# Kernel optimization log

Measured on AMD Instinct MI355X. Metric: run time of the kernel, lower is better.

Reference implementation:

```python
import jax, jax.numpy as jnp
import numpy as np

M = 8192  # output rows (size[0])


def setup_inputs() -> dict:
    key = jax.random.key(0)
    k1, k2, k3 = jax.random.split(key, 3)
    nnz = 2097152
    ids = jax.random.randint(k1, (2, nnz), 0, 8192, dtype=jnp.int64)  # [2, nnz] COO (row, col)
    vals = jax.random.normal(k2, (nnz,), dtype=jnp.float32) * 0.02
    x = jax.random.normal(k3, (8192, 128), dtype=jnp.float32)  # [N, B]
    return {"ids": ids, "vals": vals, "x": x}


def reference(ids, vals, x):
    # torch.sparse.mm(W, x) with W = coo(ids, vals, (M, N)).coalesce():
    # coalescing sums duplicate (row, col) entries, which segment_sum also does,
    # so the math is identical without explicitly deduplicating.
    rows = ids[0]  # [nnz]
    cols = ids[1]  # [nnz]
    contrib = vals[:, None] * x[cols]               # [nnz, B] gather + scale
    out = jax.ops.segment_sum(contrib, rows, num_segments=M)  # [M, B] scatter-add
    return out
```

## Files before the change

kernel.cpp:

```cpp
#include <hip/hip_runtime.h>
#include <hip/hip_bf16.h>


#define M_ROWS 8192
#define B_COLS 128
#define NG   256
#define CHK  8192
#define NBK  512
#define CAP  5120

__device__ inline unsigned int f2bf(float f) {
    unsigned int u = __float_as_uint(f);
    return (u + 0x7fffu + ((u >> 16) & 1u)) >> 16;
}
__global__ void __launch_bounds__(256) convx_kernel(const float* __restrict__ x,
                                                    uint4* __restrict__ xb) {
    int i = blockIdx.x * 256 + threadIdx.x;
    const float4* p = (const float4*)x + (size_t)i * 2;
    float4 a = p[0], b = p[1];
    uint4 o;
    o.x = f2bf(a.x) | (f2bf(a.y) << 16);
    o.y = f2bf(a.z) | (f2bf(a.w) << 16);
    o.z = f2bf(b.x) | (f2bf(b.y) << 16);
    o.w = f2bf(b.z) | (f2bf(b.w) << 16);
    xb[i] = o;
}

__global__ void __launch_bounds__(256) histT_kernel(const int* __restrict__ rows, int nnz,
                                                    int* __restrict__ perHistT) {
    __shared__ int h[NBK];
    int t = threadIdx.x, g = blockIdx.x;
    for (int i = t; i < NBK; i += 256) h[i] = 0;
    __syncthreads();
    int s = g * CHK, e = min(s + CHK, nnz);
    for (int i = s + t; i < e; i += 256) atomicAdd(&h[rows[i] >> 4], 1);
    __syncthreads();
    for (int b = t; b < NBK; b += 256) perHistT[(size_t)b * NG + g] = h[b];
}

__global__ void __launch_bounds__(512) chunkscan_kernel(int* __restrict__ perHistT,
                                                        int* __restrict__ totals) {
    int wave = threadIdx.x >> 6, lane = threadIdx.x & 63;
    int b = blockIdx.x * 8 + wave;
    int4* p = (int4*)(perHistT + (size_t)b * NG) + lane;
    int4 c = *p;
    int s = c.x + c.y + c.z + c.w;
    int incl = s;
#pragma unroll
    for (int d = 1; d < 64; d <<= 1) {
        int up = __shfl_up(incl, d, 64);
        if (lane >= d) incl += up;
    }
    int base = incl - s;
    int4 o;
    o.x = base;
    o.y = base + c.x;
    o.z = o.y + c.y;
    o.w = o.z + c.z;
    *p = o;
    if (lane == 63) totals[b] = incl;
}

__global__ void __launch_bounds__(512) scanbk_kernel(const int* __restrict__ totals, int nnz,
                                                     int* __restrict__ bucketStart) {
    __shared__ int tsh[NBK];
    __shared__ int gbase[64];
    int b = threadIdx.x;
    tsh[b] = totals[b];
    __syncthreads();
    if (b < 64) {
        int gs = 0;
#pragma unroll
        for (int k = 0; k < 8; ++k) gs += tsh[b * 8 + k];
        gbase[b] = gs;
    }
    __syncthreads();
    if (b == 0) {
        int acc = 0;
        for (int i = 0; i < 64; ++i) { int c = gbase[i]; gbase[i] = acc; acc += c; }
    }
    __syncthreads();
    int off = gbase[b >> 3];
    for (int k = (b & ~7); k < b; ++k) off += tsh[k];
    bucketStart[b] = off;
    if (b == 0) bucketStart[NBK] = nnz;
}

__global__ void __launch_bounds__(1024) scatter_kernel(const int* __restrict__ rows,
                                                       const int* __restrict__ cols,
                                                       const float* __restrict__ vals,
                                                       int nnz,
                                                       const int* __restrict__ perHistT,
                                                       const int* __restrict__ bucketStart,
                                                       int2* __restrict__ pairs) {
    __shared__ int2 stage[CHK];
    __shared__ int hist[NBK];
    __shared__ int binStart[NBK];
    __shared__ int destB[NBK];
    __shared__ int gbase[64];
    int t = threadIdx.x, g = blockIdx.x;
    int s = g * CHK, e = min(s + CHK, nnz);
    int cnt = e - s;

    int   rr[CHK / 1024];
    int   cc[CHK / 1024];
    float vv[CHK / 1024];
    for (int i = t; i < NBK; i += 1024) hist[i] = 0;
    __syncthreads();
#pragma unroll
    for (int k = 0; k < CHK / 1024; ++k) {
        int i = s + t + k * 1024;
        if (i < e) {
            rr[k] = rows[i];
            cc[k] = cols[i];
            vv[k] = vals[i];
            atomicAdd(&hist[rr[k] >> 4], 1);
        } else rr[k] = -1;
    }
    __syncthreads();
    if (t < 64) {
        int gs = 0;
#pragma unroll
        for (int k = 0; k < 8; ++k) gs += hist[t * 8 + k];
        gbase[t] = gs;
    }
    __syncthreads();
    if (t == 0) {
        int acc = 0;
        for (int i = 0; i < 64; ++i) { int c = gbase[i]; gbase[i] = acc; acc += c; }
    }
    __syncthreads();
    if (t < NBK) {
        int off = gbase[t >> 3];
        for (int k = (t & ~7); k < t; ++k) off += hist[k];
        binStart[t] = off;
        destB[t] = bucketStart[t] + perHistT[(size_t)t * NG + g] - off;
    }
    __syncthreads();
    if (t < NBK) hist[t] = binStart[t];
    __syncthreads();
#pragma unroll
    for (int k = 0; k < CHK / 1024; ++k) {
        if (rr[k] >= 0) {
            int pos = atomicAdd(&hist[rr[k] >> 4], 1);
            stage[pos] = make_int2((rr[k] << 13) | cc[k], __float_as_int(vv[k]));
        }
    }
    __syncthreads();
#pragma unroll
    for (int k = 0; k < CHK / 1024; ++k) {
        int i = t + k * 1024;
        if (i < cnt) {
            int2 en = stage[i];
            int b = en.x >> 17;
            pairs[destB[b] + i] = make_int2(en.x & 0x1FFFF, en.y);
        }
    }
}

__global__ void __launch_bounds__(1024) sortspmm_kernel(const int2* __restrict__ pairs,
                                                        const int* __restrict__ bucketStart,
                                                        const unsigned short* __restrict__ xb,
                                                        float* __restrict__ out) {
    __shared__ int2 sorted[CAP];
    __shared__ int h16w[16 * 16];
    __shared__ int h16tot[16];
    __shared__ int rs[17];
    int t = threadIdx.x;
    int bkt = blockIdx.x;
    int segS = bucketStart[bkt];
    int n = bucketStart[bkt + 1] - segS;
    int nc = min(n, CAP);
    int wave = t >> 6, lane = t & 63;
    if (t < 256) h16w[t] = 0;
    __syncthreads();

    int2 buf[5];
#pragma unroll
    for (int k = 0; k < 5; ++k) {
        int i = t + 1024 * k;
        if (i < nc) {
            long long m = __builtin_nontemporal_load((const long long*)pairs + (segS + i));
            int2 en;
            en.x = (int)m;
            en.y = (int)(m >> 32);
            buf[k] = en;
            atomicAdd(&h16w[wave * 16 + ((en.x >> 13) & 15)], 1);
        }
    }
    __syncthreads();
    if (t < 16) {
        int acc = 0;
#pragma unroll
        for (int w = 0; w < 16; ++w) {
            int c = h16w[w * 16 + t];
            h16w[w * 16 + t] = acc;
            acc += c;
        }
        h16tot[t] = acc;
    }
    __syncthreads();
    if (t == 0) {
        int acc = 0;
#pragma unroll
        for (int j = 0; j < 16; ++j) { rs[j] = acc; acc += h16tot[j]; }
        rs[16] = acc;
    }
    __syncthreads();
    if (t < 256) {
        int w = t >> 4, b = t & 15;
        h16w[t] = rs[b] + h16w[w * 16 + b];
    }
    __syncthreads();
#pragma unroll
    for (int k = 0; k < 5; ++k) {
        int i = t + 1024 * k;
        if (i < nc) {
            int2 en = buf[k];
            int pos = atomicAdd(&h16w[wave * 16 + ((en.x >> 13) & 15)], 1);
            sorted[pos] = make_int2(en.x & 8191, en.y);
        }
    }
    __syncthreads();

    int g = lane >> 4, l16 = lane & 15;
    const unsigned short* xbl = xb + l16 * 8;
    int b0 = rs[wave], e0 = rs[wave + 1];
    float acc[8];
#pragma unroll
    for (int k = 0; k < 8; ++k) acc[k] = 0.f;

    for (int i = b0; i < e0; i += 16) {
        int i0 = i + g, i1 = i0 + 4, i2 = i0 + 8, i3 = i0 + 12;
        int2 ea = (i0 < e0) ? sorted[i0] : make_int2(0, 0);
        int2 eb = (i1 < e0) ? sorted[i1] : make_int2(0, 0);
        int2 ec = (i2 < e0) ? sorted[i2] : make_int2(0, 0);
        int2 ed = (i3 < e0) ? sorted[i3] : make_int2(0, 0);
        float va = (i0 < e0) ? __int_as_float(ea.y) : 0.f;
        float vb = (i1 < e0) ? __int_as_float(eb.y) : 0.f;
        float vc = (i2 < e0) ? __int_as_float(ec.y) : 0.f;
        float vd = (i3 < e0) ? __int_as_float(ed.y) : 0.f;
        const uint4 qa = *(const uint4*)(xbl + (size_t)ea.x * B_COLS);
        const uint4 qb = *(const uint4*)(xbl + (size_t)eb.x * B_COLS);
        const uint4 qc = *(const uint4*)(xbl + (size_t)ec.x * B_COLS);
        const uint4 qd = *(const uint4*)(xbl + (size_t)ed.x * B_COLS);
#pragma unroll
        for (int k = 0; k < 4; ++k) {
            unsigned int w = (&qa.x)[k];
            acc[2 * k]     = fmaf(va, __uint_as_float(w << 16), acc[2 * k]);
            acc[2 * k + 1] = fmaf(va, __uint_as_float(w & 0xffff0000u), acc[2 * k + 1]);
        }
#pragma unroll
        for (int k = 0; k < 4; ++k) {
            unsigned int w = (&qb.x)[k];
            acc[2 * k]     = fmaf(vb, __uint_as_float(w << 16), acc[2 * k]);
            acc[2 * k + 1] = fmaf(vb, __uint_as_float(w & 0xffff0000u), acc[2 * k + 1]);
        }
#pragma unroll
        for (int k = 0; k < 4; ++k) {
            unsigned int w = (&qc.x)[k];
            acc[2 * k]     = fmaf(vc, __uint_as_float(w << 16), acc[2 * k]);
            acc[2 * k + 1] = fmaf(vc, __uint_as_float(w & 0xffff0000u), acc[2 * k + 1]);
        }
#pragma unroll
        for (int k = 0; k < 4; ++k) {
            unsigned int w = (&qd.x)[k];
            acc[2 * k]     = fmaf(vd, __uint_as_float(w << 16), acc[2 * k]);
            acc[2 * k + 1] = fmaf(vd, __uint_as_float(w & 0xffff0000u), acc[2 * k + 1]);
        }
    }
    for (int i = CAP; i < n; ++i) {
        int2 en = pairs[segS + i];
        if (((en.x >> 13) & 15) == wave) {
            float v = (g == 0) ? __int_as_float(en.y) : 0.f;
            const uint4 q = *(const uint4*)(xbl + (size_t)(en.x & 8191) * B_COLS);
#pragma unroll
            for (int k = 0; k < 4; ++k) {
                unsigned int w = (&q.x)[k];
                acc[2 * k]     = fmaf(v, __uint_as_float(w << 16), acc[2 * k]);
                acc[2 * k + 1] = fmaf(v, __uint_as_float(w & 0xffff0000u), acc[2 * k + 1]);
            }
        }
    }
#pragma unroll
    for (int k = 0; k < 8; ++k) {
        acc[k] += __shfl_xor(acc[k], 16, 64);
        acc[k] += __shfl_xor(acc[k], 32, 64);
    }
    if (lane < 16) {
        float* op = out + ((size_t)(bkt * 16 + wave)) * B_COLS + l16 * 8;
        *(float4*)op       = make_float4(acc[0], acc[1], acc[2], acc[3]);
        *((float4*)op + 1) = make_float4(acc[4], acc[5], acc[6], acc[7]);
    }
}

__global__ void atomic_spmm_kernel(const int* __restrict__ rows, const int* __restrict__ cols,
                                   const float* __restrict__ vals, int nnz,
                                   const float* __restrict__ x, float* __restrict__ out) {
    long long tid = (long long)blockIdx.x * blockDim.x + threadIdx.x;
    int e = (int)(tid >> 5);
    int g = (int)(tid & 31);
    if (e < nnz) {
        int r = rows[e], c = cols[e];
        float v = vals[e];
        const float4 xv = *(const float4*)(x + (size_t)c * B_COLS + g * 4);
        float* o = out + (size_t)r * B_COLS + g * 4;
        atomicAdd(o + 0, v * xv.x);
        atomicAdd(o + 1, v * xv.y);
        atomicAdd(o + 2, v * xv.z);
        atomicAdd(o + 3, v * xv.w);
    }
}

extern "C" void kernel_launch(void* const* d_in, const int* in_sizes, int n_in,
                              void* d_out, int out_size, void* d_ws, size_t ws_size,
                              hipStream_t stream) {
    const int*   ids  = (const int*)d_in[0];
    const int    nnz  = in_sizes[0] / 2;
    const int*   rows = ids;
    const int*   cols = ids + nnz;
    const float* vals = (const float*)d_in[1];
    const float* x    = (const float*)d_in[2];
    float*       out  = (float*)d_out;

    size_t o_perHistT    = 0;
    size_t o_totals      = o_perHistT + (size_t)NBK * NG;
    size_t o_bucketStart = o_totals + NBK;
    size_t o_xbf         = (o_bucketStart + (NBK + 1) + 3) & ~(size_t)3;
    size_t o_pairs       = o_xbf + (size_t)M_ROWS * B_COLS / 2;
    size_t need_bytes    = (o_pairs + (size_t)nnz * 2) * 4;
    int ngrid = (nnz + CHK - 1) / CHK;

    if (ws_size >= need_bytes && ngrid == NG) {
        int*            perHistT    = (int*)d_ws + o_perHistT;
        int*            totals      = (int*)d_ws + o_totals;
        int*            bucketStart = (int*)d_ws + o_bucketStart;
        unsigned short* xbf         = (unsigned short*)((int*)d_ws + o_xbf);
        int2*           pairs       = (int2*)((int*)d_ws + o_pairs);

        convx_kernel<<<(M_ROWS * B_COLS / 8) / 256, 256, 0, stream>>>(x, (uint4*)xbf);
        histT_kernel<<<NG, 256, 0, stream>>>(rows, nnz, perHistT);
        chunkscan_kernel<<<NBK / 8, 512, 0, stream>>>(perHistT, totals);
        scanbk_kernel<<<1, 512, 0, stream>>>(totals, nnz, bucketStart);
        scatter_kernel<<<NG, 1024, 0, stream>>>(rows, cols, vals, nnz,
                                                perHistT, bucketStart, pairs);
        sortspmm_kernel<<<NBK, 1024, 0, stream>>>(pairs, bucketStart, xbf, out);
    } else {
        hipMemsetAsync(d_out, 0, (size_t)out_size * sizeof(float), stream);
        long long total = (long long)nnz * 32;
        atomic_spmm_kernel<<<(unsigned)((total + 255) / 256), 256, 0, stream>>>(rows, cols, vals, nnz, x, out);
    }
}
```

Before: 128.1 us.

## Pack COO entries into 32-bit words with bf16 values and use 8-row buckets

Each intermediate (row-in-bucket, col, value) entry is packed into one 32-bit word, with the value rounded to bf16, which halves the pairs buffer traffic between the scatter and spmm kernels. Buckets shrink from 16 rows to 8 rows, doubling the bucket count and using 512-thread spmm blocks with half the shared-memory capacity. This trades value precision (bf16 instead of fp32 weights) and a smaller per-block cap, which pushes more work onto the slow overflow path for dense buckets, for reduced memory bandwidth and better occupancy.

```diff
diff --git a/kernel.cpp b/kernel.cpp
--- a/kernel.cpp
+++ b/kernel.cpp
@@ -6,13 +6,14 @@
 #define B_COLS 128
 #define NG   256
 #define CHK  8192
-#define NBK  512
-#define CAP  5120
+#define NBK  1024
+#define CAP  2560
 
 __device__ inline unsigned int f2bf(float f) {
     unsigned int u = __float_as_uint(f);
-    return (u + 0x7fffu + ((u >> 16) & 1u)) >> 16;
-}
+    return ((u + 0x7fffu + ((u >> 16) & 1u)) >> 16) & 0xFFFFu;
+}
+
 __global__ void __launch_bounds__(256) convx_kernel(const float* __restrict__ x,
                                                     uint4* __restrict__ xb) {
     int i = blockIdx.x * 256 + threadIdx.x;
@@ -33,7 +34,7 @@
     for (int i = t; i < NBK; i += 256) h[i] = 0;
     __syncthreads();
     int s = g * CHK, e = min(s + CHK, nnz);
-    for (int i = s + t; i < e; i += 256) atomicAdd(&h[rows[i] >> 4], 1);
+    for (int i = s + t; i < e; i += 256) atomicAdd(&h[rows[i] >> 3], 1);
     __syncthreads();
     for (int b = t; b < NBK; b += 256) perHistT[(size_t)b * NG + g] = h[b];
 }
@@ -61,8 +62,8 @@
     if (lane == 63) totals[b] = incl;
 }
 
-__global__ void __launch_bounds__(512) scanbk_kernel(const int* __restrict__ totals, int nnz,
-                                                     int* __restrict__ bucketStart) {
+__global__ void __launch_bounds__(1024) scanbk_kernel(const int* __restrict__ totals, int nnz,
+                                                      int* __restrict__ bucketStart) {
     __shared__ int tsh[NBK];
     __shared__ int gbase[64];
     int b = threadIdx.x;
@@ -71,7 +72,7 @@
     if (b < 64) {
         int gs = 0;
 #pragma unroll
-        for (int k = 0; k < 8; ++k) gs += tsh[b * 8 + k];
+        for (int k = 0; k < 16; ++k) gs += tsh[b * 16 + k];
         gbase[b] = gs;
     }
     __syncthreads();
@@ -80,8 +81,8 @@
         for (int i = 0; i < 64; ++i) { int c = gbase[i]; gbase[i] = acc; acc += c; }
     }
     __syncthreads();
-    int off = gbase[b >> 3];
-    for (int k = (b & ~7); k < b; ++k) off += tsh[k];
+    int off = gbase[b >> 4];
+    for (int k = (b & ~15); k < b; ++k) off += tsh[k];
     bucketStart[b] = off;
     if (b == 0) bucketStart[NBK] = nnz;
 }
@@ -92,7 +93,7 @@
                                                        int nnz,
                                                        const int* __restrict__ perHistT,
                                                        const int* __restrict__ bucketStart,
-                                                       int2* __restrict__ pairs) {
+                                                       unsigned int* __restrict__ pairs) {
     __shared__ int2 stage[CHK];
     __shared__ int hist[NBK];
     __shared__ int binStart[NBK];
@@ -114,14 +115,14 @@
             rr[k] = rows[i];
             cc[k] = cols[i];
             vv[k] = vals[i];
-            atomicAdd(&hist[rr[k] >> 4], 1);
+            atomicAdd(&hist[rr[k] >> 3], 1);
         } else rr[k] = -1;
     }
     __syncthreads();
     if (t < 64) {
         int gs = 0;
 #pragma unroll
-        for (int k = 0; k < 8; ++k) gs += hist[t * 8 + k];
+        for (int k = 0; k < 16; ++k) gs += hist[t * 16 + k];
         gbase[t] = gs;
     }
     __syncthreads();
@@ -130,19 +131,19 @@
         for (int i = 0; i < 64; ++i) { int c = gbase[i]; gbase[i] = acc; acc += c; }
     }
     __syncthreads();
-    if (t < NBK) {
-        int off = gbase[t >> 3];
-        for (int k = (t & ~7); k < t; ++k) off += hist[k];
+    {
+        int off = gbase[t >> 4];
+        for (int k = (t & ~15); k < t; ++k) off += hist[k];
         binStart[t] = off;
         destB[t] = bucketStart[t] + perHistT[(size_t)t * NG + g] - off;
     }
     __syncthreads();
-    if (t < NBK) hist[t] = binStart[t];
+    hist[t] = binStart[t];
     __syncthreads();
 #pragma unroll
     for (int k = 0; k < CHK / 1024; ++k) {
         if (rr[k] >= 0) {
-            int pos = atomicAdd(&hist[rr[k] >> 4], 1);
+            int pos = atomicAdd(&hist[rr[k] >> 3], 1);
             stage[pos] = make_int2((rr[k] << 13) | cc[k], __float_as_int(vv[k]));
         }
     }
@@ -152,73 +153,73 @@
         int i = t + k * 1024;
         if (i < cnt) {
             int2 en = stage[i];
-            int b = en.x >> 17;
-            pairs[destB[b] + i] = make_int2(en.x & 0x1FFFF, en.y);
-        }
-    }
-}
-
-__global__ void __launch_bounds__(1024) sortspmm_kernel(const int2* __restrict__ pairs,
-                                                        const int* __restrict__ bucketStart,
-                                                        const unsigned short* __restrict__ xb,
-                                                        float* __restrict__ out) {
-    __shared__ int2 sorted[CAP];
-    __shared__ int h16w[16 * 16];
-    __shared__ int h16tot[16];
-    __shared__ int rs[17];
+            int b = en.x >> 16;
+            unsigned int rowInB = ((unsigned int)en.x >> 13) & 7u;
+            unsigned int col    = (unsigned int)en.x & 0x1FFFu;
+            unsigned int packed = (rowInB << 29) | (col << 16) | f2bf(__int_as_float(en.y));
+            pairs[destB[b] + i] = packed;
+        }
+    }
+}
+
+__global__ void __launch_bounds__(512) sortspmm_kernel(const unsigned int* __restrict__ pairs,
+                                                       const int* __restrict__ bucketStart,
+                                                       const unsigned short* __restrict__ xb,
+                                                       float* __restrict__ out) {
+    __shared__ unsigned int sorted[CAP];
+    __shared__ int h8w[8 * 8];
+    __shared__ int h8tot[8];
+    __shared__ int rs[9];
     int t = threadIdx.x;
     int bkt = blockIdx.x;
     int segS = bucketStart[bkt];
     int n = bucketStart[bkt + 1] - segS;
     int nc = min(n, CAP);
     int wave = t >> 6, lane = t & 63;
-    if (t < 256) h16w[t] = 0;
-    __syncthreads();
-
-    int2 buf[5];
+    if (t < 64) h8w[t] = 0;
+    __syncthreads();
+
+    unsigned int buf[5];
 #pragma unroll
     for (int k = 0; k < 5; ++k) {
-        int i = t + 1024 * k;
+        int i = t + 512 * k;
         if (i < nc) {
-            long long m = __builtin_nontemporal_load((const long long*)pairs + (segS + i));
-            int2 en;
-            en.x = (int)m;
-            en.y = (int)(m >> 32);
+            unsigned int en = __builtin_nontemporal_load(pairs + (segS + i));
             buf[k] = en;
-            atomicAdd(&h16w[wave * 16 + ((en.x >> 13) & 15)], 1);
-        }
-    }
-    __syncthreads();
-    if (t < 16) {
+            atomicAdd(&h8w[wave * 8 + (en >> 29)], 1);
+        }
+    }
+    __syncthreads();
+    if (t < 8) {
         int acc = 0;
 #pragma unroll
-        for (int w = 0; w < 16; ++w) {
-            int c = h16w[w * 16 + t];
-            h16w[w * 16 + t] = acc;
+        for (int w = 0; w < 8; ++w) {
+            int c = h8w[w * 8 + t];
+            h8w[w * 8 + t] = acc;
             acc += c;
         }
-        h16tot[t] = acc;
+        h8tot[t] = acc;
     }
     __syncthreads();
     if (t == 0) {
         int acc = 0;
 #pragma unroll
-        for (int j = 0; j < 16; ++j) { rs[j] = acc; acc += h16tot[j]; }
-        rs[16] = acc;
-    }
-    __syncthreads();
-    if (t < 256) {
-        int w = t >> 4, b = t & 15;
-        h16w[t] = rs[b] + h16w[w * 16 + b];
+        for (int j = 0; j < 8; ++j) { rs[j] = acc; acc += h8tot[j]; }
+        rs[8] = acc;
+    }
+    __syncthreads();
+    if (t < 64) {
+        int b = t & 7;
+        h8w[t] = rs[b] + h8w[t];
     }
     __syncthreads();
 #pragma unroll
     for (int k = 0; k < 5; ++k) {
-        int i = t + 1024 * k;
+        int i = t + 512 * k;
         if (i < nc) {
-            int2 en = buf[k];
-            int pos = atomicAdd(&h16w[wave * 16 + ((en.x >> 13) & 15)], 1);
-            sorted[pos] = make_int2(en.x & 8191, en.y);
+            unsigned int en = buf[k];
+            int pos = atomicAdd(&h8w[wave * 8 + (en >> 29)], 1);
+            sorted[pos] = en;
         }
     }
     __syncthreads();
@@ -232,18 +233,18 @@
 
     for (int i = b0; i < e0; i += 16) {
         int i0 = i + g, i1 = i0 + 4, i2 = i0 + 8, i3 = i0 + 12;
-        int2 ea = (i0 < e0) ? sorted[i0] : make_int2(0, 0);
-        int2 eb = (i1 < e0) ? sorted[i1] : make_int2(0, 0);
-        int2 ec = (i2 < e0) ? sorted[i2] : make_int2(0, 0);
-        int2 ed = (i3 < e0) ? sorted[i3] : make_int2(0, 0);
-        float va = (i0 < e0) ? __int_as_float(ea.y) : 0.f;
-        float vb = (i1 < e0) ? __int_as_float(eb.y) : 0.f;
-        float vc = (i2 < e0) ? __int_as_float(ec.y) : 0.f;
-        float vd = (i3 < e0) ? __int_as_float(ed.y) : 0.f;
-        const uint4 qa = *(const uint4*)(xbl + (size_t)ea.x * B_COLS);
-        const uint4 qb = *(const uint4*)(xbl + (size_t)eb.x * B_COLS);
-        const uint4 qc = *(const uint4*)(xbl + (size_t)ec.x * B_COLS);
-        const uint4 qd = *(const uint4*)(xbl + (size_t)ed.x * B_COLS);
+        unsigned int ea = (i0 < e0) ? sorted[i0] : 0u;
+        unsigned int eb = (i1 < e0) ? sorted[i1] : 0u;
+        unsigned int ec = (i2 < e0) ? sorted[i2] : 0u;
+        unsigned int ed = (i3 < e0) ? sorted[i3] : 0u;
+        float va = __uint_as_float(ea << 16);
+        float vb = __uint_as_float(eb << 16);
+        float vc = __uint_as_float(ec << 16);
+        float vd = __uint_as_float(ed << 16);
+        const uint4 qa = *(const uint4*)(xbl + (size_t)((ea >> 16) & 0x1FFFu) * B_COLS);
+        const uint4 qb = *(const uint4*)(xbl + (size_t)((eb >> 16) & 0x1FFFu) * B_COLS);
+        const uint4 qc = *(const uint4*)(xbl + (size_t)((ec >> 16) & 0x1FFFu) * B_COLS);
+        const uint4 qd = *(const uint4*)(xbl + (size_t)((ed >> 16) & 0x1FFFu) * B_COLS);
 #pragma unroll
         for (int k = 0; k < 4; ++k) {
             unsigned int w = (&qa.x)[k];
@@ -270,10 +271,10 @@
         }
     }
     for (int i = CAP; i < n; ++i) {
-        int2 en = pairs[segS + i];
-        if (((en.x >> 13) & 15) == wave) {
-            float v = (g == 0) ? __int_as_float(en.y) : 0.f;
-            const uint4 q = *(const uint4*)(xbl + (size_t)(en.x & 8191) * B_COLS);
+        unsigned int en = pairs[segS + i];
+        if ((int)(en >> 29) == wave) {
+            float v = (g == 0) ? __uint_as_float(en << 16) : 0.f;
+            const uint4 q = *(const uint4*)(xbl + (size_t)((en >> 16) & 0x1FFFu) * B_COLS);
 #pragma unroll
             for (int k = 0; k < 4; ++k) {
                 unsigned int w = (&q.x)[k];
@@ -288,7 +289,7 @@
         acc[k] += __shfl_xor(acc[k], 32, 64);
     }
     if (lane < 16) {
-        float* op = out + ((size_t)(bkt * 16 + wave)) * B_COLS + l16 * 8;
+        float* op = out + ((size_t)(bkt * 8 + wave)) * B_COLS + l16 * 8;
         *(float4*)op       = make_float4(acc[0], acc[1], acc[2], acc[3]);
         *((float4*)op + 1) = make_float4(acc[4], acc[5], acc[6], acc[7]);
     }
@@ -328,7 +329,7 @@
     size_t o_bucketStart = o_totals + NBK;
     size_t o_xbf         = (o_bucketStart + (NBK + 1) + 3) & ~(size_t)3;
     size_t o_pairs       = o_xbf + (size_t)M_ROWS * B_COLS / 2;
-    size_t need_bytes    = (o_pairs + (size_t)nnz * 2) * 4;
+    size_t need_bytes    = (o_pairs + (size_t)nnz) * 4;
     int ngrid = (nnz + CHK - 1) / CHK;
 
     if (ws_size >= need_bytes && ngrid == NG) {
@@ -336,15 +337,15 @@
         int*            totals      = (int*)d_ws + o_totals;
         int*            bucketStart = (int*)d_ws + o_bucketStart;
         unsigned short* xbf         = (unsigned short*)((int*)d_ws + o_xbf);
-        int2*           pairs       = (int2*)((int*)d_ws + o_pairs);
+        unsigned int*   pairs       = (unsigned int*)((int*)d_ws + o_pairs);
 
         convx_kernel<<<(M_ROWS * B_COLS / 8) / 256, 256, 0, stream>>>(x, (uint4*)xbf);
         histT_kernel<<<NG, 256, 0, stream>>>(rows, nnz, perHistT);
         chunkscan_kernel<<<NBK / 8, 512, 0, stream>>>(perHistT, totals);
-        scanbk_kernel<<<1, 512, 0, stream>>>(totals, nnz, bucketStart);
+        scanbk_kernel<<<1, 1024, 0, stream>>>(totals, nnz, bucketStart);
         scatter_kernel<<<NG, 1024, 0, stream>>>(rows, cols, vals, nnz,
                                                 perHistT, bucketStart, pairs);
-        sortspmm_kernel<<<NBK, 1024, 0, stream>>>(pairs, bucketStart, xbf, out);
+        sortspmm_kernel<<<NBK, 512, 0, stream>>>(pairs, bucketStart, xbf, out);
     } else {
         hipMemsetAsync(d_out, 0, (size_t)out_size * sizeof(float), stream);
         long long total = (long long)nnz * 32;
```

Result: slower. 132.4 us (+3.4%).

## Replace global bucket scatter with per-chunk local sort and run-indexed gather

Applied to the files above, without the earlier changes.

Drops the separate histogram and two prefix-scan kernels. Each chunk is now sorted locally and written contiguously, with per-chunk bin offsets published to global memory. The SpMM kernel builds a prefix over the 256 runs belonging to its bucket and fetches entries by binary search across those runs. This removes three launches and the extra pass over rows, and makes the scatter writes contiguous. In exchange, each bucket's reads become 256 short segments with an 8-step shared-memory binary search per element, and the stored keys keep the full packed bits.

```diff
diff --git a/kernel.cpp b/kernel.cpp
--- a/kernel.cpp
+++ b/kernel.cpp
@@ -11,7 +11,7 @@
 
 __device__ inline unsigned int f2bf(float f) {
     unsigned int u = __float_as_uint(f);
-    return (u + 0x7fffu + ((u >> 16) & 1u)) >> 16;
+    return ((u + 0x7fffu + ((u >> 16) & 1u)) >> 16) & 0xFFFFu;
 }
 __global__ void __launch_bounds__(256) convx_kernel(const float* __restrict__ x,
                                                     uint4* __restrict__ xb) {
@@ -26,77 +26,15 @@
     xb[i] = o;
 }
 
-__global__ void __launch_bounds__(256) histT_kernel(const int* __restrict__ rows, int nnz,
-                                                    int* __restrict__ perHistT) {
-    __shared__ int h[NBK];
-    int t = threadIdx.x, g = blockIdx.x;
-    for (int i = t; i < NBK; i += 256) h[i] = 0;
-    __syncthreads();
-    int s = g * CHK, e = min(s + CHK, nnz);
-    for (int i = s + t; i < e; i += 256) atomicAdd(&h[rows[i] >> 4], 1);
-    __syncthreads();
-    for (int b = t; b < NBK; b += 256) perHistT[(size_t)b * NG + g] = h[b];
-}
-
-__global__ void __launch_bounds__(512) chunkscan_kernel(int* __restrict__ perHistT,
-                                                        int* __restrict__ totals) {
-    int wave = threadIdx.x >> 6, lane = threadIdx.x & 63;
-    int b = blockIdx.x * 8 + wave;
-    int4* p = (int4*)(perHistT + (size_t)b * NG) + lane;
-    int4 c = *p;
-    int s = c.x + c.y + c.z + c.w;
-    int incl = s;
-#pragma unroll
-    for (int d = 1; d < 64; d <<= 1) {
-        int up = __shfl_up(incl, d, 64);
-        if (lane >= d) incl += up;
-    }
-    int base = incl - s;
-    int4 o;
-    o.x = base;
-    o.y = base + c.x;
-    o.z = o.y + c.y;
-    o.w = o.z + c.z;
-    *p = o;
-    if (lane == 63) totals[b] = incl;
-}
-
-__global__ void __launch_bounds__(512) scanbk_kernel(const int* __restrict__ totals, int nnz,
-                                                     int* __restrict__ bucketStart) {
-    __shared__ int tsh[NBK];
-    __shared__ int gbase[64];
-    int b = threadIdx.x;
-    tsh[b] = totals[b];
-    __syncthreads();
-    if (b < 64) {
-        int gs = 0;
-#pragma unroll
-        for (int k = 0; k < 8; ++k) gs += tsh[b * 8 + k];
-        gbase[b] = gs;
-    }
-    __syncthreads();
-    if (b == 0) {
-        int acc = 0;
-        for (int i = 0; i < 64; ++i) { int c = gbase[i]; gbase[i] = acc; acc += c; }
-    }
-    __syncthreads();
-    int off = gbase[b >> 3];
-    for (int k = (b & ~7); k < b; ++k) off += tsh[k];
-    bucketStart[b] = off;
-    if (b == 0) bucketStart[NBK] = nnz;
-}
-
-__global__ void __launch_bounds__(1024) scatter_kernel(const int* __restrict__ rows,
-                                                       const int* __restrict__ cols,
-                                                       const float* __restrict__ vals,
-                                                       int nnz,
-                                                       const int* __restrict__ perHistT,
-                                                       const int* __restrict__ bucketStart,
-                                                       int2* __restrict__ pairs) {
+__global__ void __launch_bounds__(1024) chunksort_kernel(const int* __restrict__ rows,
+                                                         const int* __restrict__ cols,
+                                                         const float* __restrict__ vals,
+                                                         int nnz,
+                                                         int* __restrict__ binStartT,
+                                                         int2* __restrict__ pairs) {
     __shared__ int2 stage[CHK];
     __shared__ int hist[NBK];
     __shared__ int binStart[NBK];
-    __shared__ int destB[NBK];
     __shared__ int gbase[64];
     int t = threadIdx.x, g = blockIdx.x;
     int s = g * CHK, e = min(s + CHK, nnz);
@@ -134,7 +72,7 @@
         int off = gbase[t >> 3];
         for (int k = (t & ~7); k < t; ++k) off += hist[k];
         binStart[t] = off;
-        destB[t] = bucketStart[t] + perHistT[(size_t)t * NG + g] - off;
+        binStartT[(size_t)t * NG + g] = off;
     }
     __syncthreads();
     if (t < NBK) hist[t] = binStart[t];
@@ -150,40 +88,75 @@
 #pragma unroll
     for (int k = 0; k < CHK / 1024; ++k) {
         int i = t + k * 1024;
-        if (i < cnt) {
-            int2 en = stage[i];
-            int b = en.x >> 17;
-            pairs[destB[b] + i] = make_int2(en.x & 0x1FFFF, en.y);
-        }
-    }
-}
-
-__global__ void __launch_bounds__(1024) sortspmm_kernel(const int2* __restrict__ pairs,
-                                                        const int* __restrict__ bucketStart,
-                                                        const unsigned short* __restrict__ xb,
-                                                        float* __restrict__ out) {
+        if (i < cnt) pairs[s + i] = stage[i];
+    }
+}
+
+__global__ void __launch_bounds__(1024) bucketspmm_kernel(const int2* __restrict__ pairs,
+                                                          const int* __restrict__ binStartT,
+                                                          int nnz,
+                                                          const unsigned short* __restrict__ xb,
+                                                          float* __restrict__ out) {
     __shared__ int2 sorted[CAP];
+    __shared__ int runPrefix[NG + 1];
+    __shared__ int runAddr[NG];
+    __shared__ int gb16[16];
     __shared__ int h16w[16 * 16];
     __shared__ int h16tot[16];
     __shared__ int rs[17];
     int t = threadIdx.x;
     int bkt = blockIdx.x;
-    int segS = bucketStart[bkt];
-    int n = bucketStart[bkt + 1] - segS;
+    int wave = t >> 6, lane = t & 63;
+
+    if (t < NG) {
+        int g = t;
+        int st = binStartT[(size_t)bkt * NG + g];
+        int en;
+        if (bkt == NBK - 1) en = min(CHK, nnz - g * CHK);
+        else                en = binStartT[(size_t)(bkt + 1) * NG + g];
+        runAddr[g] = g * CHK + st;
+        runPrefix[g] = en - st;
+    }
+    if (t < 256) h16w[t] = 0;
+    __syncthreads();
+    if (t < 16) {
+        int gs = 0;
+#pragma unroll
+        for (int k = 0; k < 16; ++k) gs += runPrefix[t * 16 + k];
+        gb16[t] = gs;
+    }
+    __syncthreads();
+    if (t == 0) {
+        int acc = 0;
+        for (int i = 0; i < 16; ++i) { int c = gb16[i]; gb16[i] = acc; acc += c; }
+    }
+    __syncthreads();
+    int myoff = 0, mylen = 0;
+    if (t < NG) {
+        mylen = runPrefix[t];
+        myoff = gb16[t >> 4];
+        for (int k = (t & ~15); k < t; ++k) myoff += runPrefix[k];
+    }
+    __syncthreads();
+    if (t < NG) runPrefix[t] = myoff;
+    if (t == NG - 1) runPrefix[NG] = myoff + mylen;
+    __syncthreads();
+
+    int n = runPrefix[NG];
     int nc = min(n, CAP);
-    int wave = t >> 6, lane = t & 63;
-    if (t < 256) h16w[t] = 0;
-    __syncthreads();
 
     int2 buf[5];
 #pragma unroll
     for (int k = 0; k < 5; ++k) {
         int i = t + 1024 * k;
         if (i < nc) {
-            long long m = __builtin_nontemporal_load((const long long*)pairs + (segS + i));
-            int2 en;
-            en.x = (int)m;
-            en.y = (int)(m >> 32);
+            int lo = 0, hi = NG - 1;
+#pragma unroll
+            for (int st8 = 0; st8 < 8; ++st8) {
+                int mid = (lo + hi + 1) >> 1;
+                if (runPrefix[mid] <= i) lo = mid; else hi = mid - 1;
+            }
+            int2 en = pairs[runAddr[lo] + (i - runPrefix[lo])];
             buf[k] = en;
             atomicAdd(&h16w[wave * 16 + ((en.x >> 13) & 15)], 1);
         }
@@ -270,7 +243,12 @@
         }
     }
     for (int i = CAP; i < n; ++i) {
-        int2 en = pairs[segS + i];
+        int lo = 0, hi = NG - 1;
+        for (int st8 = 0; st8 < 8; ++st8) {
+            int mid = (lo + hi + 1) >> 1;
+            if (runPrefix[mid] <= i) lo = mid; else hi = mid - 1;
+        }
+        int2 en = pairs[runAddr[lo] + (i - runPrefix[lo])];
         if (((en.x >> 13) & 15) == wave) {
             float v = (g == 0) ? __int_as_float(en.y) : 0.f;
             const uint4 q = *(const uint4*)(xbl + (size_t)(en.x & 8191) * B_COLS);
@@ -323,28 +301,20 @@
     const float* x    = (const float*)d_in[2];
     float*       out  = (float*)d_out;
 
-    size_t o_perHistT    = 0;
-    size_t o_totals      = o_perHistT + (size_t)NBK * NG;
-    size_t o_bucketStart = o_totals + NBK;
-    size_t o_xbf         = (o_bucketStart + (NBK + 1) + 3) & ~(size_t)3;
-    size_t o_pairs       = o_xbf + (size_t)M_ROWS * B_COLS / 2;
-    size_t need_bytes    = (o_pairs + (size_t)nnz * 2) * 4;
+    size_t o_binStartT = 0;
+    size_t o_xbf       = (o_binStartT + (size_t)NBK * NG + 3) & ~(size_t)3;
+    size_t o_pairs     = o_xbf + (size_t)M_ROWS * B_COLS / 2;
+    size_t need_bytes  = (o_pairs + (size_t)nnz * 2) * 4;
     int ngrid = (nnz + CHK - 1) / CHK;
 
     if (ws_size >= need_bytes && ngrid == NG) {
-        int*            perHistT    = (int*)d_ws + o_perHistT;
-        int*            totals      = (int*)d_ws + o_totals;
-        int*            bucketStart = (int*)d_ws + o_bucketStart;
-        unsigned short* xbf         = (unsigned short*)((int*)d_ws + o_xbf);
-        int2*           pairs       = (int2*)((int*)d_ws + o_pairs);
+        int*            binStartT = (int*)d_ws + o_binStartT;
+        unsigned short* xbf       = (unsigned short*)((int*)d_ws + o_xbf);
+        int2*           pairs     = (int2*)((int*)d_ws + o_pairs);
 
         convx_kernel<<<(M_ROWS * B_COLS / 8) / 256, 256, 0, stream>>>(x, (uint4*)xbf);
-        histT_kernel<<<NG, 256, 0, stream>>>(rows, nnz, perHistT);
-        chunkscan_kernel<<<NBK / 8, 512, 0, stream>>>(perHistT, totals);
-        scanbk_kernel<<<1, 512, 0, stream>>>(totals, nnz, bucketStart);
-        scatter_kernel<<<NG, 1024, 0, stream>>>(rows, cols, vals, nnz,
-                                                perHistT, bucketStart, pairs);
-        sortspmm_kernel<<<NBK, 1024, 0, stream>>>(pairs, bucketStart, xbf, out);
+        chunksort_kernel<<<NG, 1024, 0, stream>>>(rows, cols, vals, nnz, binStartT, pairs);
+        bucketspmm_kernel<<<NBK, 1024, 0, stream>>>(pairs, binStartT, nnz, xbf, out);
     } else {
         hipMemsetAsync(d_out, 0, (size_t)out_size * sizeof(float), stream);
         long long total = (long long)nnz * 32;
```

Measured after the change: 111.9 us. 12.6% less time.
